# Optimization experiments

Hardware: AMD Instinct MI355X
Metric: run time of the kernel (lower is better)

## Reference

```python
import jax, jax.numpy as jnp
import numpy as np

N_NODES = 50000
N_EDGES = 1000000
H_DIM = 128
OUT_DIM = 64
N_RELS = 16  # num_bases == num_rels


def setup_inputs() -> dict:
    key = jax.random.key(0)
    ks = jax.random.split(key, 12)
    node_ids = jnp.arange(N_NODES, dtype=jnp.int64) if jax.config.jax_enable_x64 else jnp.arange(N_NODES, dtype=jnp.int32)
    src = jax.random.randint(ks[0], (N_EDGES,), 0, N_NODES)
    dst = jax.random.randint(ks[1], (N_EDGES,), 0, N_NODES)
    etype = jax.random.randint(ks[2], (N_EDGES,), 0, N_RELS)
    norm = jax.random.uniform(ks[3], (N_EDGES, 1), dtype=jnp.float32)
    s1 = 1.0 / np.sqrt(H_DIM)
    s2 = 1.0 / np.sqrt(OUT_DIM)
    emb = jax.random.normal(ks[4], (N_NODES, H_DIM), dtype=jnp.float32)
    V1 = jax.random.normal(ks[5], (N_RELS, H_DIM, H_DIM), dtype=jnp.float32) * s1
    comp1 = jax.random.normal(ks[6], (N_RELS, N_RELS), dtype=jnp.float32) * (1.0 / np.sqrt(N_RELS))
    bias1 = jnp.zeros((H_DIM,), dtype=jnp.float32)
    V2 = jax.random.normal(ks[7], (N_RELS, H_DIM, OUT_DIM), dtype=jnp.float32) * s2
    comp2 = jax.random.normal(ks[8], (N_RELS, N_RELS), dtype=jnp.float32) * (1.0 / np.sqrt(N_RELS))
    bias2 = jnp.zeros((OUT_DIM,), dtype=jnp.float32)
    return {"node_ids": node_ids, "src": src, "dst": dst, "etype": etype, "norm": norm,
            "emb": emb, "V1": V1, "comp1": comp1, "bias1": bias1,
            "V2": V2, "comp2": comp2, "bias2": bias2}


def _rel_graph_conv(x, src, dst, etype, norm, V, comp, bias, num_nodes):
    # Basis decomposition: W_r = sum_b comp[r, b] * V_b  -> [R, in, out]
    W = jnp.einsum('rb,bio->rio', comp, V)
    # Per-relation transform of all nodes: [R, N, out]
    Y = jnp.einsum('ni,rio->rno', x, W)
    # Per-edge message: gather (etype, src) then scale by norm  -> [E, out]
    m = Y[etype, src] * norm
    # Scatter-add to destination nodes
    h = jax.ops.segment_sum(m, dst, num_segments=num_nodes)
    return h + bias


def reference(node_ids, src, dst, etype, norm, emb, V1, comp1, bias1, V2, comp2, bias2):
    x = emb[node_ids]  # [N, H]
    h = jax.nn.relu(_rel_graph_conv(x, src, dst, etype, norm, V1, comp1, bias1, x.shape[0]))
    h = _rel_graph_conv(h, src, dst, etype, norm, V2, comp2, bias2, x.shape[0])
    return h
```

## Files before the change

### kernel.cpp

```cpp
#include <hip/hip_runtime.h>


typedef short bf16x8 __attribute__((ext_vector_type(8)));
typedef float f32x4 __attribute__((ext_vector_type(4)));

#define RELS 16
#define HDIM 128
#define DSTBLK 50
#define MT_P 4
#define CHUNK 32

__device__ inline unsigned short f2bf(float f) {
  unsigned int u = __float_as_uint(f);
  unsigned int r = u + 0x7FFFu + ((u >> 16) & 1u);
  return (unsigned short)(r >> 16);
}

__global__ void cvt_bf16(const float* __restrict__ in, unsigned short* __restrict__ out, int n8) {
  int i = blockIdx.x * blockDim.x + threadIdx.x;
  if (i >= n8) return;
  float4 a = ((const float4*)in)[i * 2];
  float4 b = ((const float4*)in)[i * 2 + 1];
  uint4 o;
  o.x = (unsigned)f2bf(a.x) | ((unsigned)f2bf(a.y) << 16);
  o.y = (unsigned)f2bf(a.z) | ((unsigned)f2bf(a.w) << 16);
  o.z = (unsigned)f2bf(b.x) | ((unsigned)f2bf(b.y) << 16);
  o.w = (unsigned)f2bf(b.z) | ((unsigned)f2bf(b.w) << 16);
  ((uint4*)out)[i] = o;
}

__global__ void compute_w(const float* __restrict__ comp, const float* __restrict__ V,
                          unsigned short* __restrict__ Wt, int IO) {
  int idx = blockIdx.x * blockDim.x + threadIdx.x;
  if (idx >= RELS * IO * HDIM) return;
  int k = idx & (HDIM - 1);
  int o = (idx >> 7) % IO;
  int r = idx / (IO * HDIM);
  float s = 0.f;
#pragma unroll
  for (int b = 0; b < RELS; b++)
    s = fmaf(comp[r * RELS + b], V[(size_t)b * HDIM * IO + (size_t)k * IO + o], s);
  Wt[idx] = f2bf(s);
}

__global__ void hist_bins(const int* __restrict__ dst, const int* __restrict__ etype,
                          int n, int nbins, int* __restrict__ counts) {
  __shared__ int lh[16000];
  for (int j = threadIdx.x; j < nbins; j += blockDim.x) lh[j] = 0;
  __syncthreads();
  for (int i = blockIdx.x * blockDim.x + threadIdx.x; i < n; i += gridDim.x * blockDim.x)
    atomicAdd(&lh[(dst[i] / DSTBLK) * RELS + etype[i]], 1);
  __syncthreads();
  for (int j = threadIdx.x; j < nbins; j += blockDim.x) {
    int c = lh[j];
    if (c) atomicAdd(&counts[j], c);
  }
}

__global__ void scan_offsets(const int* __restrict__ counts, int* __restrict__ offsets, int nbins) {
  __shared__ int csum[257];
  const int t = threadIdx.x;
  const int CH = (nbins + 255) / 256;
  int lo = t * CH, hi = min(lo + CH, nbins);
  int s = 0;
  for (int i = lo; i < hi; i++) s += (counts[i] + 15) & ~15;
  csum[t + 1] = s;
  if (t == 0) csum[0] = 0;
  __syncthreads();
  if (t == 0)
    for (int i = 1; i <= 256; i++) csum[i] += csum[i - 1];
  __syncthreads();
  int run = csum[t];
  for (int i = lo; i < hi; i++) {
    offsets[i] = run;
    run += (counts[i] + 15) & ~15;
  }
  if (lo < hi && hi == nbins) offsets[nbins] = run;
}

__global__ void scatter_bins(const int* __restrict__ src, const int* __restrict__ dst,
                             const int* __restrict__ etype, const float* __restrict__ norm,
                             int n, const int* __restrict__ offsets, int* __restrict__ cursor,
                             uint2* __restrict__ ebuf) {
  for (int i = blockIdx.x * blockDim.x + threadIdx.x; i < n; i += gridDim.x * blockDim.x) {
    int d = dst[i];
    int blk = d / DSTBLK;
    int b = blk * RELS + etype[i];
    int p = offsets[b] + atomicAdd(&cursor[b], 1);
    ebuf[p] = make_uint2((unsigned)src[i] | ((unsigned)(d - blk * DSTBLK) << 20),
                         __float_as_uint(norm[i]));
  }
}

template <int OUT, bool BF16_RELU_OUT>
__launch_bounds__(256, 4)
__global__ void rgcn_layer(const unsigned short* __restrict__ Xb,
                           const unsigned short* __restrict__ Wt,
                           const uint2* __restrict__ ebuf,
                           const int* __restrict__ offsets, const int* __restrict__ counts,
                           const float* __restrict__ bias, void* __restrict__ Hout,
                           int nNodes) {
  constexpr int NT = OUT / 64;
  __shared__ __align__(16) unsigned short xs[CHUNK][136];
  __shared__ __align__(16) unsigned short ys[OUT][40];
  __shared__ __align__(16) unsigned short pmat[64][40];

  const int t = threadIdx.x;
  const int w = t >> 6;
  const int lane = t & 63;
  const int quad = lane >> 4;
  const int l16 = lane & 15;
  const bool isHandler = (t & 7) == 0;
  const int myCol = t >> 3;
  const int nodeBase = blockIdx.x * DSTBLK;
  const int binBase = blockIdx.x * RELS;
  const int colBase = w * (OUT / 4);

  for (int i = t; i < CHUNK * 136 / 8; i += 256) ((uint4*)xs)[i] = make_uint4(0, 0, 0, 0);
  for (int i = t; i < OUT * 40 / 8; i += 256) ((uint4*)ys)[i] = make_uint4(0, 0, 0, 0);
  for (int i = t; i < 64 * 40 / 8; i += 256) ((uint4*)pmat)[i] = make_uint4(0, 0, 0, 0);

  f32x4 pacc[MT_P][NT] = {};
  bool prevValid = false;
  int prevDloc = 0;

  for (int r = 0; r < RELS; r++) {
    const int start = offsets[binBase + r];
    const int end = offsets[binBase + r + 1];
    if (start >= end) continue;
    const int realEnd = start + counts[binBase + r];

    const unsigned short* Wr = Wt + (size_t)r * OUT * HDIM;
    bf16x8 wf[4][NT];
#pragma unroll
    for (int ks = 0; ks < 4; ks++)
#pragma unroll
      for (int nt = 0; nt < NT; nt++)
        wf[ks][nt] = *(const bf16x8*)(Wr + (size_t)(colBase + nt * 16 + l16) * HDIM + ks * 32 + quad * 8);

    for (int base = start; base < end; base += CHUNK) {
      const int nRows = min(CHUNK, realEnd - base);

      __syncthreads();

#pragma unroll
      for (int i = 0; i < 2; i++) {
        int idx = i * 256 + t;
        int row = idx >> 4, k8 = idx & 15;
        if (row < nRows) {
          int s = (int)(ebuf[base + row].x & 0xFFFFFu);
          *(uint4*)&xs[row][k8 * 8] = *(const uint4*)(Xb + (size_t)s * HDIM + k8 * 8);
        }
      }
      if (isHandler) {
        if (prevValid) pmat[prevDloc][myCol] = 0;
        if (myCol < nRows) {
          uint2 md = ebuf[base + myCol];
          int dl = (int)(md.x >> 20) & 63;
          pmat[dl][myCol] = f2bf(__uint_as_float(md.y));
          prevDloc = dl;
          prevValid = true;
        } else {
          prevValid = false;
        }
      }

      __syncthreads();

#pragma unroll
      for (int mt = 0; mt < 2; mt++) {
        if (mt * 16 < nRows) {
          f32x4 dacc[NT] = {};
#pragma unroll
          for (int ks = 0; ks < 4; ks++) {
            bf16x8 a = *(const bf16x8*)&xs[mt * 16 + l16][ks * 32 + quad * 8];
#pragma unroll
            for (int nt = 0; nt < NT; nt++)
              dacc[nt] = __builtin_amdgcn_mfma_f32_16x16x32_bf16(a, wf[ks][nt], dacc[nt], 0, 0, 0);
          }
#pragma unroll
          for (int nt = 0; nt < NT; nt++) {
            uint2 pk;
            pk.x = (unsigned)f2bf(dacc[nt][0]) | ((unsigned)f2bf(dacc[nt][1]) << 16);
            pk.y = (unsigned)f2bf(dacc[nt][2]) | ((unsigned)f2bf(dacc[nt][3]) << 16);
            *(uint2*)&ys[colBase + nt * 16 + l16][mt * 16 + quad * 4] = pk;
          }
        }
      }

      {
        bf16x8 bfv[NT];
#pragma unroll
        for (int nt = 0; nt < NT; nt++)
          bfv[nt] = *(const bf16x8*)&ys[colBase + nt * 16 + l16][quad * 8];
#pragma unroll
        for (int mt = 0; mt < MT_P; mt++) {
          bf16x8 a = *(const bf16x8*)&pmat[mt * 16 + l16][quad * 8];
#pragma unroll
          for (int nt = 0; nt < NT; nt++)
            pacc[mt][nt] = __builtin_amdgcn_mfma_f32_16x16x32_bf16(a, bfv[nt], pacc[mt][nt], 0, 0, 0);
        }
      }
    }
  }

#pragma unroll
  for (int mt = 0; mt < MT_P; mt++) {
#pragma unroll
    for (int reg = 0; reg < 4; reg++) {
      int ld = mt * 16 + quad * 4 + reg;
      int node = nodeBase + ld;
      if (ld < DSTBLK && node < nNodes) {
#pragma unroll
        for (int nt = 0; nt < NT; nt++) {
          int col = colBase + nt * 16 + l16;
          float v = pacc[mt][nt][reg] + bias[col];
          if constexpr (BF16_RELU_OUT)
            ((unsigned short*)Hout)[(size_t)node * OUT + col] = f2bf(fmaxf(v, 0.f));
          else
            ((float*)Hout)[(size_t)node * OUT + col] = v;
        }
      }
    }
  }
}

extern "C" void kernel_launch(void* const* d_in, const int* in_sizes, int n_in,
                              void* d_out, int out_size, void* d_ws, size_t ws_size,
                              hipStream_t stream) {
  const int*   src   = (const int*)d_in[1];
  const int*   dst   = (const int*)d_in[2];
  const int*   etype = (const int*)d_in[3];
  const float* norm  = (const float*)d_in[4];
  const float* emb   = (const float*)d_in[5];
  const float* V1    = (const float*)d_in[6];
  const float* comp1 = (const float*)d_in[7];
  const float* bias1 = (const float*)d_in[8];
  const float* V2    = (const float*)d_in[9];
  const float* comp2 = (const float*)d_in[10];
  const float* bias2 = (const float*)d_in[11];
  float* out = (float*)d_out;

  const int N = in_sizes[0];
  const int E = in_sizes[1];
  const int H = 128, O = 64;
  const int NB = (N + DSTBLK - 1) / DSTBLK;
  const int NBINS = NB * RELS;
  const int EPAD_MAX = E + NBINS * 16;

  char* ws = (char*)d_ws;
  size_t off = 0;
  auto alloc = [&](size_t bytes) -> void* {
    void* p = ws + off;
    off += (bytes + 255) & ~(size_t)255;
    return p;
  };
  unsigned short* W1t  = (unsigned short*)alloc(sizeof(short) * RELS * H * H);
  unsigned short* W2t  = (unsigned short*)alloc(sizeof(short) * RELS * O * H);
  unsigned short* embh = (unsigned short*)alloc(sizeof(short) * (size_t)N * H);
  unsigned short* h1b  = (unsigned short*)alloc(sizeof(short) * (size_t)N * H);
  uint2* ebuf = (uint2*)alloc(sizeof(uint2) * EPAD_MAX);
  int* counts  = (int*)alloc(sizeof(int) * NBINS);
  int* cursor  = (int*)alloc(sizeof(int) * NBINS);
  int* offsets = (int*)alloc(sizeof(int) * (NBINS + 1));

  hipMemsetAsync(counts, 0, sizeof(int) * NBINS, stream);
  hipMemsetAsync(cursor, 0, sizeof(int) * NBINS, stream);

  cvt_bf16<<<((size_t)N * H / 8 + 255) / 256, 256, 0, stream>>>(emb, embh, N * H / 8);
  compute_w<<<(RELS * H * H + 255) / 256, 256, 0, stream>>>(comp1, V1, W1t, H);
  compute_w<<<(RELS * O * H + 255) / 256, 256, 0, stream>>>(comp2, V2, W2t, O);
  hist_bins<<<1024, 256, 0, stream>>>(dst, etype, E, NBINS, counts);
  scan_offsets<<<1, 256, 0, stream>>>(counts, offsets, NBINS);
  scatter_bins<<<1024, 256, 0, stream>>>(src, dst, etype, norm, E, offsets, cursor, ebuf);

  rgcn_layer<128, true><<<NB, 256, 0, stream>>>(embh, W1t, ebuf, offsets, counts, bias1, (void*)h1b, N);
  rgcn_layer<64, false><<<NB, 256, 0, stream>>>(h1b, W2t, ebuf, offsets, counts, bias2, (void*)out, N);
}
```

Baseline: 476.2 us.

## Double-buffer edge gathers in RGCN layer and enlarge destination blocks

Restructures the RGCN layer loop into a flattened, software-pipelined schedule. The next chunk's edge metadata and source-row gathers are issued before the current chunk's MFMA work, and the results are written into a second LDS buffer, so one barrier per chunk replaces two. The destination block grows from 50 to 66 nodes with a fifth M tile, and launch bounds drop to 3 waves per SIMD to make room for the extra registers and LDS. Also switches the offset scan to a parallel Hillis-Steele scan, shrinks the histogram grid, and cuts the histogram shared memory to fit the new bin count. The risks are lower occupancy and extra register pressure from holding the prefetched data.

```diff
diff --git a/kernel.cpp b/kernel.cpp
--- a/kernel.cpp
+++ b/kernel.cpp
@@ -6,9 +6,10 @@
 
 #define RELS 16
 #define HDIM 128
-#define DSTBLK 50
-#define MT_P 4
+#define DSTBLK 66
+#define MT_P 5
 #define CHUNK 32
+#define MAXBINS 12288
 
 __device__ inline unsigned short f2bf(float f) {
   unsigned int u = __float_as_uint(f);
@@ -45,7 +46,7 @@
 
 __global__ void hist_bins(const int* __restrict__ dst, const int* __restrict__ etype,
                           int n, int nbins, int* __restrict__ counts) {
-  __shared__ int lh[16000];
+  __shared__ int lh[MAXBINS];
   for (int j = threadIdx.x; j < nbins; j += blockDim.x) lh[j] = 0;
   __syncthreads();
   for (int i = blockIdx.x * blockDim.x + threadIdx.x; i < n; i += gridDim.x * blockDim.x)
@@ -58,24 +59,27 @@
 }
 
 __global__ void scan_offsets(const int* __restrict__ counts, int* __restrict__ offsets, int nbins) {
-  __shared__ int csum[257];
+  __shared__ int csum[256];
   const int t = threadIdx.x;
   const int CH = (nbins + 255) / 256;
   int lo = t * CH, hi = min(lo + CH, nbins);
   int s = 0;
   for (int i = lo; i < hi; i++) s += (counts[i] + 15) & ~15;
-  csum[t + 1] = s;
-  if (t == 0) csum[0] = 0;
-  __syncthreads();
-  if (t == 0)
-    for (int i = 1; i <= 256; i++) csum[i] += csum[i - 1];
-  __syncthreads();
-  int run = csum[t];
+  csum[t] = s;
+  __syncthreads();
+#pragma unroll
+  for (int d = 1; d < 256; d <<= 1) {
+    int v = (t >= d) ? csum[t - d] : 0;
+    __syncthreads();
+    csum[t] += v;
+    __syncthreads();
+  }
+  int run = (t == 0) ? 0 : csum[t - 1];
   for (int i = lo; i < hi; i++) {
     offsets[i] = run;
     run += (counts[i] + 15) & ~15;
   }
-  if (lo < hi && hi == nbins) offsets[nbins] = run;
+  if (lo < nbins && hi == nbins) offsets[nbins] = run;
 }
 
 __global__ void scatter_bins(const int* __restrict__ src, const int* __restrict__ dst,
@@ -93,7 +97,7 @@
 }
 
 template <int OUT, bool BF16_RELU_OUT>
-__launch_bounds__(256, 4)
+__launch_bounds__(256, 3)
 __global__ void rgcn_layer(const unsigned short* __restrict__ Xb,
                            const unsigned short* __restrict__ Wt,
                            const uint2* __restrict__ ebuf,
@@ -101,107 +105,154 @@
                            const float* __restrict__ bias, void* __restrict__ Hout,
                            int nNodes) {
   constexpr int NT = OUT / 64;
-  __shared__ __align__(16) unsigned short xs[CHUNK][136];
+  __shared__ __align__(16) unsigned short xs[2][CHUNK][136];
   __shared__ __align__(16) unsigned short ys[OUT][40];
-  __shared__ __align__(16) unsigned short pmat[64][40];
+  __shared__ __align__(16) unsigned short pmat[2][80][40];
 
   const int t = threadIdx.x;
   const int w = t >> 6;
   const int lane = t & 63;
   const int quad = lane >> 4;
   const int l16 = lane & 15;
+  const int r0 = t >> 4;
+  const int k8 = t & 15;
   const bool isHandler = (t & 7) == 0;
   const int myCol = t >> 3;
   const int nodeBase = blockIdx.x * DSTBLK;
   const int binBase = blockIdx.x * RELS;
   const int colBase = w * (OUT / 4);
 
-  for (int i = t; i < CHUNK * 136 / 8; i += 256) ((uint4*)xs)[i] = make_uint4(0, 0, 0, 0);
+  for (int i = t; i < 2 * CHUNK * 136 / 8; i += 256) ((uint4*)xs)[i] = make_uint4(0, 0, 0, 0);
   for (int i = t; i < OUT * 40 / 8; i += 256) ((uint4*)ys)[i] = make_uint4(0, 0, 0, 0);
-  for (int i = t; i < 64 * 40 / 8; i += 256) ((uint4*)pmat)[i] = make_uint4(0, 0, 0, 0);
+  for (int i = t; i < 2 * 80 * 40 / 8; i += 256) ((uint4*)pmat)[i] = make_uint4(0, 0, 0, 0);
 
   f32x4 pacc[MT_P][NT] = {};
-  bool prevValid = false;
-  int prevDloc = 0;
-
-  for (int r = 0; r < RELS; r++) {
-    const int start = offsets[binBase + r];
-    const int end = offsets[binBase + r + 1];
-    if (start >= end) continue;
-    const int realEnd = start + counts[binBase + r];
-
-    const unsigned short* Wr = Wt + (size_t)r * OUT * HDIM;
-    bf16x8 wf[4][NT];
-#pragma unroll
-    for (int ks = 0; ks < 4; ks++)
+
+  int bin = 0, base = 0, binEnd = 0, realEnd = 0;
+  for (; bin < RELS; bin++) {
+    base = offsets[binBase + bin];
+    binEnd = offsets[binBase + bin + 1];
+    if (base < binEnd) { realEnd = base + counts[binBase + bin]; break; }
+  }
+
+  __syncthreads();
+
+  int pdA = -1, pdB = -1;
+  if (bin < RELS) {
+    int nR = min(CHUNK, realEnd - base);
+    if (r0 < nR) {
+      uint2 e = ebuf[base + r0];
+      *(uint4*)&xs[0][r0][k8 * 8] = *(const uint4*)(Xb + (size_t)(e.x & 0xFFFFFu) * HDIM + k8 * 8);
+    }
+    if (16 + r0 < nR) {
+      uint2 e = ebuf[base + 16 + r0];
+      *(uint4*)&xs[0][16 + r0][k8 * 8] = *(const uint4*)(Xb + (size_t)(e.x & 0xFFFFFu) * HDIM + k8 * 8);
+    }
+    if (isHandler && myCol < nR) {
+      uint2 m = ebuf[base + myCol];
+      int dl = (int)(m.x >> 20) & 127;
+      pmat[0][dl][myCol] = f2bf(__uint_as_float(m.y));
+      pdB = dl;
+    }
+  }
+  __syncthreads();
+
+  int cb = 0;
+  int curRel = -1;
+  bf16x8 wf[4][NT];
+
+  while (bin < RELS) {
+    const int nRows = min(CHUNK, realEnd - base);
+
+    if (bin != curRel) {
+      curRel = bin;
+      const unsigned short* Wr = Wt + (size_t)bin * OUT * HDIM;
+#pragma unroll
+      for (int ks = 0; ks < 4; ks++)
+#pragma unroll
+        for (int nt = 0; nt < NT; nt++)
+          wf[ks][nt] = *(const bf16x8*)(Wr + (size_t)(colBase + nt * 16 + l16) * HDIM + ks * 32 + quad * 8);
+    }
+
+    int nbin = bin, nbase = base + CHUNK, nbinEnd = binEnd, nrealEnd = realEnd;
+    if (nbase >= binEnd) {
+      for (nbin = bin + 1; nbin < RELS; nbin++) {
+        nbase = offsets[binBase + nbin];
+        nbinEnd = offsets[binBase + nbin + 1];
+        if (nbase < nbinEnd) { nrealEnd = nbase + counts[binBase + nbin]; break; }
+      }
+    }
+    const bool hasNext = nbin < RELS;
+    const int nR = hasNext ? min(CHUNK, nrealEnd - nbase) : 0;
+
+    uint2 e0, e1, em;
+    if (hasNext) {
+      if (r0 < nR) e0 = ebuf[nbase + r0];
+      if (16 + r0 < nR) e1 = ebuf[nbase + 16 + r0];
+      if (isHandler && myCol < nR) em = ebuf[nbase + myCol];
+    }
+
+#pragma unroll
+    for (int mt = 0; mt < 2; mt++) {
+      if (mt * 16 < nRows) {
+        f32x4 dacc[NT] = {};
+#pragma unroll
+        for (int ks = 0; ks < 4; ks++) {
+          bf16x8 a = *(const bf16x8*)&xs[cb][mt * 16 + l16][ks * 32 + quad * 8];
+#pragma unroll
+          for (int nt = 0; nt < NT; nt++)
+            dacc[nt] = __builtin_amdgcn_mfma_f32_16x16x32_bf16(a, wf[ks][nt], dacc[nt], 0, 0, 0);
+        }
+#pragma unroll
+        for (int nt = 0; nt < NT; nt++) {
+          uint2 pk;
+          pk.x = (unsigned)f2bf(dacc[nt][0]) | ((unsigned)f2bf(dacc[nt][1]) << 16);
+          pk.y = (unsigned)f2bf(dacc[nt][2]) | ((unsigned)f2bf(dacc[nt][3]) << 16);
+          *(uint2*)&ys[colBase + nt * 16 + l16][mt * 16 + quad * 4] = pk;
+        }
+      }
+    }
+
+    uint4 g0, g1;
+    if (hasNext) {
+      if (r0 < nR) g0 = *(const uint4*)(Xb + (size_t)(e0.x & 0xFFFFFu) * HDIM + k8 * 8);
+      if (16 + r0 < nR) g1 = *(const uint4*)(Xb + (size_t)(e1.x & 0xFFFFFu) * HDIM + k8 * 8);
+    }
+
+    {
+      bf16x8 bfv[NT];
 #pragma unroll
       for (int nt = 0; nt < NT; nt++)
-        wf[ks][nt] = *(const bf16x8*)(Wr + (size_t)(colBase + nt * 16 + l16) * HDIM + ks * 32 + quad * 8);
-
-    for (int base = start; base < end; base += CHUNK) {
-      const int nRows = min(CHUNK, realEnd - base);
-
-      __syncthreads();
-
-#pragma unroll
-      for (int i = 0; i < 2; i++) {
-        int idx = i * 256 + t;
-        int row = idx >> 4, k8 = idx & 15;
-        if (row < nRows) {
-          int s = (int)(ebuf[base + row].x & 0xFFFFFu);
-          *(uint4*)&xs[row][k8 * 8] = *(const uint4*)(Xb + (size_t)s * HDIM + k8 * 8);
+        bfv[nt] = *(const bf16x8*)&ys[colBase + nt * 16 + l16][quad * 8];
+#pragma unroll
+      for (int mt = 0; mt < MT_P; mt++) {
+        bf16x8 a = *(const bf16x8*)&pmat[cb][mt * 16 + l16][quad * 8];
+#pragma unroll
+        for (int nt = 0; nt < NT; nt++)
+          pacc[mt][nt] = __builtin_amdgcn_mfma_f32_16x16x32_bf16(a, bfv[nt], pacc[mt][nt], 0, 0, 0);
+      }
+    }
+
+    if (hasNext) {
+      if (r0 < nR) *(uint4*)&xs[cb ^ 1][r0][k8 * 8] = g0;
+      if (16 + r0 < nR) *(uint4*)&xs[cb ^ 1][16 + r0][k8 * 8] = g1;
+      if (isHandler) {
+        if (pdA >= 0) pmat[cb ^ 1][pdA][myCol] = 0;
+        if (myCol < nR) {
+          int dl = (int)(em.x >> 20) & 127;
+          pmat[cb ^ 1][dl][myCol] = f2bf(__uint_as_float(em.y));
+          pdA = dl;
+        } else {
+          pdA = -1;
         }
       }
-      if (isHandler) {
-        if (prevValid) pmat[prevDloc][myCol] = 0;
-        if (myCol < nRows) {
-          uint2 md = ebuf[base + myCol];
-          int dl = (int)(md.x >> 20) & 63;
-          pmat[dl][myCol] = f2bf(__uint_as_float(md.y));
-          prevDloc = dl;
-          prevValid = true;
-        } else {
-          prevValid = false;
-        }
-      }
-
-      __syncthreads();
-
-#pragma unroll
-      for (int mt = 0; mt < 2; mt++) {
-        if (mt * 16 < nRows) {
-          f32x4 dacc[NT] = {};
-#pragma unroll
-          for (int ks = 0; ks < 4; ks++) {
-            bf16x8 a = *(const bf16x8*)&xs[mt * 16 + l16][ks * 32 + quad * 8];
-#pragma unroll
-            for (int nt = 0; nt < NT; nt++)
-              dacc[nt] = __builtin_amdgcn_mfma_f32_16x16x32_bf16(a, wf[ks][nt], dacc[nt], 0, 0, 0);
-          }
-#pragma unroll
-          for (int nt = 0; nt < NT; nt++) {
-            uint2 pk;
-            pk.x = (unsigned)f2bf(dacc[nt][0]) | ((unsigned)f2bf(dacc[nt][1]) << 16);
-            pk.y = (unsigned)f2bf(dacc[nt][2]) | ((unsigned)f2bf(dacc[nt][3]) << 16);
-            *(uint2*)&ys[colBase + nt * 16 + l16][mt * 16 + quad * 4] = pk;
-          }
-        }
-      }
-
-      {
-        bf16x8 bfv[NT];
-#pragma unroll
-        for (int nt = 0; nt < NT; nt++)
-          bfv[nt] = *(const bf16x8*)&ys[colBase + nt * 16 + l16][quad * 8];
-#pragma unroll
-        for (int mt = 0; mt < MT_P; mt++) {
-          bf16x8 a = *(const bf16x8*)&pmat[mt * 16 + l16][quad * 8];
-#pragma unroll
-          for (int nt = 0; nt < NT; nt++)
-            pacc[mt][nt] = __builtin_amdgcn_mfma_f32_16x16x32_bf16(a, bfv[nt], pacc[mt][nt], 0, 0, 0);
-        }
-      }
-    }
+    }
+    { int tmp = pdA; pdA = pdB; pdB = tmp; }
+
+    if (hasNext) __syncthreads();
+
+    bin = nbin; base = nbase; binEnd = nbinEnd; realEnd = nrealEnd;
+    cb ^= 1;
   }
 
 #pragma unroll
@@ -270,7 +321,7 @@
   cvt_bf16<<<((size_t)N * H / 8 + 255) / 256, 256, 0, stream>>>(emb, embh, N * H / 8);
   compute_w<<<(RELS * H * H + 255) / 256, 256, 0, stream>>>(comp1, V1, W1t, H);
   compute_w<<<(RELS * O * H + 255) / 256, 256, 0, stream>>>(comp2, V2, W2t, O);
-  hist_bins<<<1024, 256, 0, stream>>>(dst, etype, E, NBINS, counts);
+  hist_bins<<<256, 256, 0, stream>>>(dst, etype, E, NBINS, counts);
   scan_offsets<<<1, 256, 0, stream>>>(counts, offsets, NBINS);
   scatter_bins<<<1024, 256, 0, stream>>>(src, dst, etype, norm, E, offsets, cursor, ebuf);
 
```

Result: faster. 460.8 us (-3.2%).

## Shrink destination blocks to 32 and build aggregation matrix in registers

Applied to the files above, without the earlier changes.

Destination blocks shrink from 50 to 32 nodes, so the per-node aggregation needs only two MFMA row tiles, and index math becomes shifts and masks. The kernel no longer stages gathered source rows and the norm matrix in shared memory: X rows are read straight from global memory into MFMA operands, and the one-hot norm matrix is built in registers by comparing packed edge records. This drops two block-wide barriers per chunk. The histogram now uses global atomics instead of a shared-memory histogram, the offset scan becomes a parallel tree scan, and norms are stored as bf16. The cost is an extra memset of the edge buffer and less reuse of gathered rows across waves.

```diff
diff --git a/kernel.cpp b/kernel.cpp
--- a/kernel.cpp
+++ b/kernel.cpp
@@ -6,8 +6,7 @@
 
 #define RELS 16
 #define HDIM 128
-#define DSTBLK 50
-#define MT_P 4
+#define DSTBLK 32
 #define CHUNK 32
 
 __device__ inline unsigned short f2bf(float f) {
@@ -44,38 +43,33 @@
 }
 
 __global__ void hist_bins(const int* __restrict__ dst, const int* __restrict__ etype,
-                          int n, int nbins, int* __restrict__ counts) {
-  __shared__ int lh[16000];
-  for (int j = threadIdx.x; j < nbins; j += blockDim.x) lh[j] = 0;
-  __syncthreads();
+                          int n, int* __restrict__ counts) {
   for (int i = blockIdx.x * blockDim.x + threadIdx.x; i < n; i += gridDim.x * blockDim.x)
-    atomicAdd(&lh[(dst[i] / DSTBLK) * RELS + etype[i]], 1);
-  __syncthreads();
-  for (int j = threadIdx.x; j < nbins; j += blockDim.x) {
-    int c = lh[j];
-    if (c) atomicAdd(&counts[j], c);
-  }
+    atomicAdd(&counts[(dst[i] >> 5) * RELS + etype[i]], 1);
 }
 
 __global__ void scan_offsets(const int* __restrict__ counts, int* __restrict__ offsets, int nbins) {
-  __shared__ int csum[257];
+  __shared__ int csum[256];
   const int t = threadIdx.x;
   const int CH = (nbins + 255) / 256;
   int lo = t * CH, hi = min(lo + CH, nbins);
   int s = 0;
   for (int i = lo; i < hi; i++) s += (counts[i] + 15) & ~15;
-  csum[t + 1] = s;
-  if (t == 0) csum[0] = 0;
+  csum[t] = s;
   __syncthreads();
-  if (t == 0)
-    for (int i = 1; i <= 256; i++) csum[i] += csum[i - 1];
-  __syncthreads();
-  int run = csum[t];
+#pragma unroll
+  for (int d = 1; d < 256; d <<= 1) {
+    int v = (t >= d) ? csum[t - d] : 0;
+    __syncthreads();
+    csum[t] += v;
+    __syncthreads();
+  }
+  int run = (t == 0) ? 0 : csum[t - 1];
   for (int i = lo; i < hi; i++) {
     offsets[i] = run;
     run += (counts[i] + 15) & ~15;
   }
-  if (lo < hi && hi == nbins) offsets[nbins] = run;
+  if (lo < nbins && hi == nbins) offsets[nbins] = run;
 }
 
 __global__ void scatter_bins(const int* __restrict__ src, const int* __restrict__ dst,
@@ -84,11 +78,10 @@
                              uint2* __restrict__ ebuf) {
   for (int i = blockIdx.x * blockDim.x + threadIdx.x; i < n; i += gridDim.x * blockDim.x) {
     int d = dst[i];
-    int blk = d / DSTBLK;
-    int b = blk * RELS + etype[i];
+    int b = (d >> 5) * RELS + etype[i];
     int p = offsets[b] + atomicAdd(&cursor[b], 1);
-    ebuf[p] = make_uint2((unsigned)src[i] | ((unsigned)(d - blk * DSTBLK) << 20),
-                         __float_as_uint(norm[i]));
+    ebuf[p] = make_uint2((unsigned)src[i] | ((unsigned)(d & 31) << 20),
+                         (unsigned)f2bf(norm[i]));
   }
 }
 
@@ -101,33 +94,28 @@
                            const float* __restrict__ bias, void* __restrict__ Hout,
                            int nNodes) {
   constexpr int NT = OUT / 64;
-  __shared__ __align__(16) unsigned short xs[CHUNK][136];
   __shared__ __align__(16) unsigned short ys[OUT][40];
-  __shared__ __align__(16) unsigned short pmat[64][40];
 
   const int t = threadIdx.x;
   const int w = t >> 6;
   const int lane = t & 63;
   const int quad = lane >> 4;
   const int l16 = lane & 15;
-  const bool isHandler = (t & 7) == 0;
-  const int myCol = t >> 3;
   const int nodeBase = blockIdx.x * DSTBLK;
   const int binBase = blockIdx.x * RELS;
   const int colBase = w * (OUT / 4);
 
-  for (int i = t; i < CHUNK * 136 / 8; i += 256) ((uint4*)xs)[i] = make_uint4(0, 0, 0, 0);
-  for (int i = t; i < OUT * 40 / 8; i += 256) ((uint4*)ys)[i] = make_uint4(0, 0, 0, 0);
-  for (int i = t; i < 64 * 40 / 8; i += 256) ((uint4*)pmat)[i] = make_uint4(0, 0, 0, 0);
-
-  f32x4 pacc[MT_P][NT] = {};
-  bool prevValid = false;
-  int prevDloc = 0;
+  {
+    uint4* yz = (uint4*)&ys[colBase][0];
+    for (int i = lane; i < (OUT / 4) * 5; i += 64) yz[i] = make_uint4(0, 0, 0, 0);
+  }
+
+  f32x4 pacc[2][NT] = {};
 
   for (int r = 0; r < RELS; r++) {
     const int start = offsets[binBase + r];
-    const int end = offsets[binBase + r + 1];
-    if (start >= end) continue;
+    const int binEnd = offsets[binBase + r + 1];
+    if (start >= binEnd) continue;
     const int realEnd = start + counts[binBase + r];
 
     const unsigned short* Wr = Wt + (size_t)r * OUT * HDIM;
@@ -138,42 +126,32 @@
       for (int nt = 0; nt < NT; nt++)
         wf[ks][nt] = *(const bf16x8*)(Wr + (size_t)(colBase + nt * 16 + l16) * HDIM + ks * 32 + quad * 8);
 
-    for (int base = start; base < end; base += CHUNK) {
-      const int nRows = min(CHUNK, realEnd - base);
-
-      __syncthreads();
-
-#pragma unroll
-      for (int i = 0; i < 2; i++) {
-        int idx = i * 256 + t;
-        int row = idx >> 4, k8 = idx & 15;
-        if (row < nRows) {
-          int s = (int)(ebuf[base + row].x & 0xFFFFFu);
-          *(uint4*)&xs[row][k8 * 8] = *(const uint4*)(Xb + (size_t)s * HDIM + k8 * 8);
-        }
-      }
-      if (isHandler) {
-        if (prevValid) pmat[prevDloc][myCol] = 0;
-        if (myCol < nRows) {
-          uint2 md = ebuf[base + myCol];
-          int dl = (int)(md.x >> 20) & 63;
-          pmat[dl][myCol] = f2bf(__uint_as_float(md.y));
-          prevDloc = dl;
-          prevValid = true;
-        } else {
-          prevValid = false;
-        }
-      }
-
-      __syncthreads();
+    for (int base = start; base < binEnd; base += CHUNK) {
+      const int nR = min(CHUNK, realEnd - base);
+      const int avail = binEnd - base;
+      const bool upper = avail > 16;
+
+      uint4 q01, q23, q45, q67;
+      if (quad * 8 < avail) {
+        const uint4* eb = (const uint4*)(ebuf + base + quad * 8);
+        q01 = eb[0]; q23 = eb[1]; q45 = eb[2]; q67 = eb[3];
+      } else {
+        q01 = q23 = q45 = q67 = make_uint4(~0u, ~0u, ~0u, ~0u);
+      }
+      uint2 er0 = ebuf[base + l16];
+      uint2 er1 = upper ? ebuf[base + 16 + l16] : make_uint2(0u, 0u);
 
 #pragma unroll
       for (int mt = 0; mt < 2; mt++) {
-        if (mt * 16 < nRows) {
+        if (mt * 16 < nR) {
+          unsigned w0 = mt ? er1.x : er0.x;
+          int row = mt * 16 + l16;
+          size_t s = (row < nR) ? (size_t)(w0 & 0xFFFFFu) : 0;
+          const unsigned short* xr = Xb + s * HDIM + quad * 8;
           f32x4 dacc[NT] = {};
 #pragma unroll
           for (int ks = 0; ks < 4; ks++) {
-            bf16x8 a = *(const bf16x8*)&xs[mt * 16 + l16][ks * 32 + quad * 8];
+            bf16x8 a = *(const bf16x8*)(xr + ks * 32);
 #pragma unroll
             for (int nt = 0; nt < NT; nt++)
               dacc[nt] = __builtin_amdgcn_mfma_f32_16x16x32_bf16(a, wf[ks][nt], dacc[nt], 0, 0, 0);
@@ -188,29 +166,36 @@
         }
       }
 
-      {
-        bf16x8 bfv[NT];
+      bf16x8 bfv[NT];
+#pragma unroll
+      for (int nt = 0; nt < NT; nt++)
+        bfv[nt] = *(const bf16x8*)&ys[colBase + nt * 16 + l16][quad * 8];
+
+#pragma unroll
+      for (int mt = 0; mt < 2; mt++) {
+        const unsigned tgt = (unsigned)(mt * 16 + l16);
+        union { unsigned u[4]; bf16x8 v; } pf;
+        pf.u[0] = ((((q01.x >> 20) & 127u) == tgt) ? (q01.y & 0xFFFFu) : 0u) |
+                  (((((q01.z >> 20) & 127u) == tgt) ? (q01.w & 0xFFFFu) : 0u) << 16);
+        pf.u[1] = ((((q23.x >> 20) & 127u) == tgt) ? (q23.y & 0xFFFFu) : 0u) |
+                  (((((q23.z >> 20) & 127u) == tgt) ? (q23.w & 0xFFFFu) : 0u) << 16);
+        pf.u[2] = ((((q45.x >> 20) & 127u) == tgt) ? (q45.y & 0xFFFFu) : 0u) |
+                  (((((q45.z >> 20) & 127u) == tgt) ? (q45.w & 0xFFFFu) : 0u) << 16);
+        pf.u[3] = ((((q67.x >> 20) & 127u) == tgt) ? (q67.y & 0xFFFFu) : 0u) |
+                  (((((q67.z >> 20) & 127u) == tgt) ? (q67.w & 0xFFFFu) : 0u) << 16);
 #pragma unroll
         for (int nt = 0; nt < NT; nt++)
-          bfv[nt] = *(const bf16x8*)&ys[colBase + nt * 16 + l16][quad * 8];
-#pragma unroll
-        for (int mt = 0; mt < MT_P; mt++) {
-          bf16x8 a = *(const bf16x8*)&pmat[mt * 16 + l16][quad * 8];
-#pragma unroll
-          for (int nt = 0; nt < NT; nt++)
-            pacc[mt][nt] = __builtin_amdgcn_mfma_f32_16x16x32_bf16(a, bfv[nt], pacc[mt][nt], 0, 0, 0);
-        }
+          pacc[mt][nt] = __builtin_amdgcn_mfma_f32_16x16x32_bf16(pf.v, bfv[nt], pacc[mt][nt], 0, 0, 0);
       }
     }
   }
 
 #pragma unroll
-  for (int mt = 0; mt < MT_P; mt++) {
+  for (int mt = 0; mt < 2; mt++) {
 #pragma unroll
     for (int reg = 0; reg < 4; reg++) {
-      int ld = mt * 16 + quad * 4 + reg;
-      int node = nodeBase + ld;
-      if (ld < DSTBLK && node < nNodes) {
+      int node = nodeBase + mt * 16 + quad * 4 + reg;
+      if (node < nNodes) {
 #pragma unroll
         for (int nt = 0; nt < NT; nt++) {
           int col = colBase + nt * 16 + l16;
@@ -246,7 +231,7 @@
   const int H = 128, O = 64;
   const int NB = (N + DSTBLK - 1) / DSTBLK;
   const int NBINS = NB * RELS;
-  const int EPAD_MAX = E + NBINS * 16;
+  const int EPAD_MAX = E + NBINS * 16 + 64;
 
   char* ws = (char*)d_ws;
   size_t off = 0;
@@ -266,11 +251,12 @@
 
   hipMemsetAsync(counts, 0, sizeof(int) * NBINS, stream);
   hipMemsetAsync(cursor, 0, sizeof(int) * NBINS, stream);
+  hipMemsetAsync(ebuf, 0xFF, sizeof(uint2) * EPAD_MAX, stream);
 
   cvt_bf16<<<((size_t)N * H / 8 + 255) / 256, 256, 0, stream>>>(emb, embh, N * H / 8);
   compute_w<<<(RELS * H * H + 255) / 256, 256, 0, stream>>>(comp1, V1, W1t, H);
   compute_w<<<(RELS * O * H + 255) / 256, 256, 0, stream>>>(comp2, V2, W2t, O);
-  hist_bins<<<1024, 256, 0, stream>>>(dst, etype, E, NBINS, counts);
+  hist_bins<<<512, 256, 0, stream>>>(dst, etype, E, counts);
   scan_offsets<<<1, 256, 0, stream>>>(counts, offsets, NBINS);
   scatter_bins<<<1024, 256, 0, stream>>>(src, dst, etype, norm, E, offsets, cursor, ebuf);
 
```

Measured after the change: 817.9 us. 71.8% more time.
